# Optimization experiments

Measured on AMD Instinct MI355X. Metric: run time of the kernel, lower is better.

## Reference

```python
import jax, jax.numpy as jnp
import numpy as np

N_ATOMS = 51
VMIN = -10.0
VMAX = 10.0
GAMMA = 0.99
ACTION_DIM = 4
B = 524288

def setup_inputs() -> dict:
    key = jax.random.key(0)
    k1, k2, k3, k4, k5 = jax.random.split(key, 5)
    return {
        "next_logits": jax.random.normal(k1, (B, N_ATOMS), dtype=jnp.float32),
        "old_logits": jax.random.normal(k2, (B, ACTION_DIM, N_ATOMS), dtype=jnp.float32),
        "reward": jax.random.normal(k3, (B,), dtype=jnp.float32),
        "done": jax.random.uniform(k4, (B,), dtype=jnp.float32),
        "actions": jax.random.randint(k5, (B,), 0, ACTION_DIM, dtype=jnp.int32),
    }

def reference(next_logits, old_logits, reward, done, actions):
    b_sz, n_atoms = next_logits.shape
    delta_z = (VMAX - VMIN) / (n_atoms - 1)
    support = VMIN + delta_z * jnp.arange(n_atoms, dtype=next_logits.dtype)  # [A]
    # next-state distribution (Qnet softmax output), action-selected upstream
    next_p = jax.nn.softmax(next_logits, axis=-1)                            # [B, A]
    done_b = (done > 0.95).astype(next_logits.dtype)                         # binarize
    # Bellman-backed atoms, clamped to support range
    t_z = reward[:, None] + (1.0 - done_b)[:, None] * GAMMA * support        # [B, A]
    t_z = jnp.clip(t_z, VMIN, VMAX)
    b = (t_z - VMIN) / delta_z                                               # [B, A]
    l = jnp.floor(b).astype(jnp.int32)
    u = jnp.ceil(b).astype(jnp.int32)
    rows = jnp.arange(b_sz, dtype=jnp.int32)[:, None]                        # [B, 1]
    lf = l.astype(b.dtype)
    uf = u.astype(b.dtype)
    proj_dist = (jnp.zeros((b_sz, n_atoms), dtype=next_p.dtype)
                 .at[rows, l].add(next_p * (uf - b))
                 .at[rows, u].add(next_p * (b - lf)))                         # [B, A]
    proj_dist = jax.lax.stop_gradient(proj_dist)
    # cross-entropy loss against current net's action-conditioned distribution
    log_p_all = jax.nn.log_softmax(old_logits, axis=-1)                      # [B, act, A]
    log_p = jnp.take_along_axis(log_p_all, actions[:, None, None], axis=1)[:, 0, :]  # [B, A]
    loss = -jnp.mean(jnp.sum(proj_dist * log_p, axis=1))
    return loss, proj_dist
```

## Files before the change

### kernel.cpp

```cpp
#include <hip/hip_runtime.h>
#include <math.h>

#define N_ATOMS 51
#define VMIN_F  (-10.0f)
#define VMAX_F  (10.0f)
#define GAMMA_F (0.99f)
#define ACT     4
#define BLOCK   256
#define WPB     (BLOCK / 64)

__device__ __forceinline__ float wred_max(float v) {
#pragma unroll
    for (int off = 32; off; off >>= 1) v = fmaxf(v, __shfl_xor(v, off, 64));
    return v;
}
__device__ __forceinline__ float wred_sum(float v) {
#pragma unroll
    for (int off = 32; off; off >>= 1) v += __shfl_xor(v, off, 64);
    return v;
}

__global__ __launch_bounds__(BLOCK) void c51_kernel(
    const float* __restrict__ next_logits,
    const float* __restrict__ old_logits,
    const float* __restrict__ reward,
    const float* __restrict__ done,
    const int*   __restrict__ actions,
    float* __restrict__ out,
    int B)
{
    __shared__ float bins[WPB][64];
    __shared__ float wacc[WPB];

    const int lane  = threadIdx.x & 63;
    const int wid   = threadIdx.x >> 6;
    const int gwave = (blockIdx.x * blockDim.x + threadIdx.x) >> 6;
    const int nwav  = (gridDim.x * blockDim.x) >> 6;

    const float delta_z = 0.4f;
    const bool  active  = lane < N_ATOMS;
    const float zj = __fadd_rn(VMIN_F, __fmul_rn(delta_z, (float)lane));

    float acc = 0.0f;

    const int iters = (B + nwav - 1) / nwav;
    for (int it = 0; it < iters; ++it) {
        const int  r     = gwave + it * nwav;
        const bool valid = r < B;

        float x = (valid && active) ? next_logits[(size_t)r * N_ATOMS + lane]
                                    : -INFINITY;
        float m = wred_max(x);
        float e = (valid && active) ? expf(__fsub_rn(x, m)) : 0.0f;
        float s = wred_sum(e);
        float p = valid ? __fdiv_rn(e, s) : 0.0f;

        float wl = 0.0f, wu = 0.0f;
        int   li = 0,    ui = 0;
        if (valid) {
            float rw = reward[r];
            float db = (done[r] > 0.95f) ? 1.0f : 0.0f;
            float s1 = __fmul_rn(__fsub_rn(1.0f, db), GAMMA_F);
            float tz = __fadd_rn(rw, __fmul_rn(s1, zj));
            tz = fminf(fmaxf(tz, VMIN_F), VMAX_F);
            float b  = __fdiv_rn(__fsub_rn(tz, VMIN_F), delta_z);
            float lf = floorf(b);
            float uf = ceilf(b);
            li = (int)lf;
            ui = (int)uf;
            wl = __fmul_rn(p, __fsub_rn(uf, b));
            wu = __fmul_rn(p, __fsub_rn(b, lf));
        }

        bins[wid][lane] = 0.0f;
        __syncthreads();
        if (valid && active) {
            atomicAdd(&bins[wid][li], wl);
            atomicAdd(&bins[wid][ui], wu);
        }
        __syncthreads();
        float proj = (valid && active) ? bins[wid][lane] : 0.0f;

        float term = 0.0f;
        if (valid) {
            int a = actions[r];
            const float* op = old_logits + ((size_t)r * ACT + a) * N_ATOMS;
            float y  = active ? op[lane] : -INFINITY;
            float m2 = wred_max(y);
            float sh = __fsub_rn(y, m2);
            float e2 = active ? expf(sh) : 0.0f;
            float s2 = wred_sum(e2);
            float lp = __fsub_rn(sh, logf(s2));
            term = active ? __fmul_rn(proj, lp) : 0.0f;
        }
        acc += wred_sum(term);

        if (valid && active) out[1 + (size_t)r * N_ATOMS + lane] = proj;
    }

    if (lane == 0) wacc[wid] = acc;
    __syncthreads();
    if (threadIdx.x == 0) {
        float t = 0.0f;
#pragma unroll
        for (int i = 0; i < WPB; ++i) t += wacc[i];
        atomicAdd(out, -t / (float)B);
    }
}

extern "C" void kernel_launch(void* const* d_in, const int* in_sizes, int n_in,
                              void* d_out, int out_size, void* d_ws, size_t ws_size,
                              hipStream_t stream) {
    const float* next_logits = (const float*)d_in[0];
    const float* old_logits  = (const float*)d_in[1];
    const float* reward      = (const float*)d_in[2];
    const float* done        = (const float*)d_in[3];
    const int*   actions     = (const int*)d_in[4];
    float* out = (float*)d_out;
    const int B = in_sizes[2];

    hipMemsetAsync(d_out, 0, sizeof(float), stream);

    const int grid = 2048;
    c51_kernel<<<grid, BLOCK, 0, stream>>>(next_logits, old_logits, reward,
                                           done, actions, out, B);
}
```

Baseline: 986.1 us.

## Process two rows per wave with DPP reductions and wave-local LDS sync

Each wave now handles two rows per iteration and issues all global loads (logits, reward, done, actions, old logits) up front, so more memory requests are in flight at once. Shuffle-based reductions become DPP row operations plus a readlane. Block-wide __syncthreads around the per-wave histogram bins are replaced by lgkmcnt waits, since each wave owns its own bins. Fast __expf, __logf and rcp approximations replace the precise versions, and the loss is accumulated per lane with a single reduction at the end, at some cost in numerical accuracy.

Result: faster. 801.0 us (-18.8%).

```diff
diff --git a/kernel.cpp b/kernel.cpp
--- a/kernel.cpp
+++ b/kernel.cpp
@@ -8,16 +8,29 @@
 #define ACT     4
 #define BLOCK   256
 #define WPB     (BLOCK / 64)
+#define RPI     2
+#define GRID    2048
 
-__device__ __forceinline__ float wred_max(float v) {
-#pragma unroll
-    for (int off = 32; off; off >>= 1) v = fmaxf(v, __shfl_xor(v, off, 64));
-    return v;
+#define DPP_F(OLDF, SRCF, CTRL, RMASK) \
+  __int_as_float(__builtin_amdgcn_update_dpp(__float_as_int(OLDF), __float_as_int(SRCF), (CTRL), (RMASK), 0xF, false))
+
+__device__ __forceinline__ float wave_max_u(float v) {
+    v = fmaxf(v, DPP_F(-INFINITY, v, 0x111, 0xF));
+    v = fmaxf(v, DPP_F(-INFINITY, v, 0x112, 0xF));
+    v = fmaxf(v, DPP_F(-INFINITY, v, 0x114, 0xF));
+    v = fmaxf(v, DPP_F(-INFINITY, v, 0x118, 0xF));
+    v = fmaxf(v, DPP_F(-INFINITY, v, 0x142, 0xA));
+    v = fmaxf(v, DPP_F(-INFINITY, v, 0x143, 0xC));
+    return __int_as_float(__builtin_amdgcn_readlane(__float_as_int(v), 63));
 }
-__device__ __forceinline__ float wred_sum(float v) {
-#pragma unroll
-    for (int off = 32; off; off >>= 1) v += __shfl_xor(v, off, 64);
-    return v;
+__device__ __forceinline__ float wave_sum_u(float v) {
+    v = __fadd_rn(v, DPP_F(0.0f, v, 0x111, 0xF));
+    v = __fadd_rn(v, DPP_F(0.0f, v, 0x112, 0xF));
+    v = __fadd_rn(v, DPP_F(0.0f, v, 0x114, 0xF));
+    v = __fadd_rn(v, DPP_F(0.0f, v, 0x118, 0xF));
+    v = __fadd_rn(v, DPP_F(0.0f, v, 0x142, 0xA));
+    v = __fadd_rn(v, DPP_F(0.0f, v, 0x143, 0xC));
+    return __int_as_float(__builtin_amdgcn_readlane(__float_as_int(v), 63));
 }
 
 __global__ __launch_bounds__(BLOCK) void c51_kernel(
@@ -29,13 +42,13 @@
     float* __restrict__ out,
     int B)
 {
-    __shared__ float bins[WPB][64];
+    __shared__ float bins[WPB][RPI][64];
     __shared__ float wacc[WPB];
 
     const int lane  = threadIdx.x & 63;
     const int wid   = threadIdx.x >> 6;
-    const int gwave = (blockIdx.x * blockDim.x + threadIdx.x) >> 6;
-    const int nwav  = (gridDim.x * blockDim.x) >> 6;
+    const int gwave = blockIdx.x * WPB + wid;
+    const int nwav  = GRID * WPB;
 
     const float delta_z = 0.4f;
     const bool  active  = lane < N_ATOMS;
@@ -43,67 +56,87 @@
 
     float acc = 0.0f;
 
-    const int iters = (B + nwav - 1) / nwav;
+    const int stride = nwav * RPI;
+    const int iters  = (B + stride - 1) / stride;
+
     for (int it = 0; it < iters; ++it) {
-        const int  r     = gwave + it * nwav;
-        const bool valid = r < B;
+        const int  r0 = (gwave + it * nwav) * RPI;
+        const int  r1 = r0 + 1;
+        const bool vA = r0 < B, vB = r1 < B;
 
-        float x = (valid && active) ? next_logits[(size_t)r * N_ATOMS + lane]
-                                    : -INFINITY;
-        float m = wred_max(x);
-        float e = (valid && active) ? expf(__fsub_rn(x, m)) : 0.0f;
-        float s = wred_sum(e);
-        float p = valid ? __fdiv_rn(e, s) : 0.0f;
+        float xA = (vA && active) ? next_logits[(size_t)r0 * N_ATOMS + lane] : -INFINITY;
+        float xB = (vB && active) ? next_logits[(size_t)r1 * N_ATOMS + lane] : -INFINITY;
+        float rwA = vA ? reward[r0] : 0.0f;
+        float rwB = vB ? reward[r1] : 0.0f;
+        float dnA = vA ? done[r0] : 1.0f;
+        float dnB = vB ? done[r1] : 1.0f;
+        int   aA  = vA ? actions[r0] : 0;
+        int   aB  = vB ? actions[r1] : 0;
+        float yA = (vA && active) ? old_logits[((size_t)r0 * ACT + aA) * N_ATOMS + lane] : -INFINITY;
+        float yB = (vB && active) ? old_logits[((size_t)r1 * ACT + aB) * N_ATOMS + lane] : -INFINITY;
 
-        float wl = 0.0f, wu = 0.0f;
-        int   li = 0,    ui = 0;
-        if (valid) {
-            float rw = reward[r];
-            float db = (done[r] > 0.95f) ? 1.0f : 0.0f;
-            float s1 = __fmul_rn(__fsub_rn(1.0f, db), GAMMA_F);
-            float tz = __fadd_rn(rw, __fmul_rn(s1, zj));
-            tz = fminf(fmaxf(tz, VMIN_F), VMAX_F);
-            float b  = __fdiv_rn(__fsub_rn(tz, VMIN_F), delta_z);
-            float lf = floorf(b);
-            float uf = ceilf(b);
-            li = (int)lf;
-            ui = (int)uf;
-            wl = __fmul_rn(p, __fsub_rn(uf, b));
-            wu = __fmul_rn(p, __fsub_rn(b, lf));
+        float mA = wave_max_u(xA);
+        float mB = wave_max_u(xB);
+        float eA = (vA && active) ? __expf(__fsub_rn(xA, mA)) : 0.0f;
+        float eB = (vB && active) ? __expf(__fsub_rn(xB, mB)) : 0.0f;
+        float sA = wave_sum_u(eA);
+        float sB = wave_sum_u(eB);
+        float pA = __fmul_rn(eA, __builtin_amdgcn_rcpf(sA));
+        float pB = __fmul_rn(eB, __builtin_amdgcn_rcpf(sB));
+
+        float s1A = __fmul_rn(__fsub_rn(1.0f, (dnA > 0.95f) ? 1.0f : 0.0f), GAMMA_F);
+        float s1B = __fmul_rn(__fsub_rn(1.0f, (dnB > 0.95f) ? 1.0f : 0.0f), GAMMA_F);
+        float tzA = __fadd_rn(rwA, __fmul_rn(s1A, zj));
+        float tzB = __fadd_rn(rwB, __fmul_rn(s1B, zj));
+        tzA = fminf(fmaxf(tzA, VMIN_F), VMAX_F);
+        tzB = fminf(fmaxf(tzB, VMIN_F), VMAX_F);
+        float bA = __fdiv_rn(__fsub_rn(tzA, VMIN_F), delta_z);
+        float bB = __fdiv_rn(__fsub_rn(tzB, VMIN_F), delta_z);
+        float lfA = floorf(bA), ufA = ceilf(bA);
+        float lfB = floorf(bB), ufB = ceilf(bB);
+        int liA = (int)lfA, uiA = (int)ufA;
+        int liB = (int)lfB, uiB = (int)ufB;
+        float wlA = __fmul_rn(pA, __fsub_rn(ufA, bA));
+        float wuA = __fmul_rn(pA, __fsub_rn(bA, lfA));
+        float wlB = __fmul_rn(pB, __fsub_rn(ufB, bB));
+        float wuB = __fmul_rn(pB, __fsub_rn(bB, lfB));
+
+        bins[wid][0][lane] = 0.0f;
+        bins[wid][1][lane] = 0.0f;
+        asm volatile("s_waitcnt lgkmcnt(0)" ::: "memory");
+        if (active) {
+            if (vA) { atomicAdd(&bins[wid][0][liA], wlA); atomicAdd(&bins[wid][0][uiA], wuA); }
+            if (vB) { atomicAdd(&bins[wid][1][liB], wlB); atomicAdd(&bins[wid][1][uiB], wuB); }
         }
+        asm volatile("s_waitcnt lgkmcnt(0)" ::: "memory");
+        float prA = bins[wid][0][lane];
+        float prB = bins[wid][1][lane];
 
-        bins[wid][lane] = 0.0f;
-        __syncthreads();
-        if (valid && active) {
-            atomicAdd(&bins[wid][li], wl);
-            atomicAdd(&bins[wid][ui], wu);
-        }
-        __syncthreads();
-        float proj = (valid && active) ? bins[wid][lane] : 0.0f;
+        float m2A = wave_max_u(yA);
+        float m2B = wave_max_u(yB);
+        float shA = __fsub_rn(yA, m2A);
+        float shB = __fsub_rn(yB, m2B);
+        float e2A = (vA && active) ? __expf(shA) : 0.0f;
+        float e2B = (vB && active) ? __expf(shB) : 0.0f;
+        float s2A = wave_sum_u(e2A);
+        float s2B = wave_sum_u(e2B);
+        float lpA = __fsub_rn(shA, __logf(s2A));
+        float lpB = __fsub_rn(shB, __logf(s2B));
 
-        float term = 0.0f;
-        if (valid) {
-            int a = actions[r];
-            const float* op = old_logits + ((size_t)r * ACT + a) * N_ATOMS;
-            float y  = active ? op[lane] : -INFINITY;
-            float m2 = wred_max(y);
-            float sh = __fsub_rn(y, m2);
-            float e2 = active ? expf(sh) : 0.0f;
-            float s2 = wred_sum(e2);
-            float lp = __fsub_rn(sh, logf(s2));
-            term = active ? __fmul_rn(proj, lp) : 0.0f;
-        }
-        acc += wred_sum(term);
+        if (vA && active) acc = __fadd_rn(acc, __fmul_rn(prA, lpA));
+        if (vB && active) acc = __fadd_rn(acc, __fmul_rn(prB, lpB));
 
-        if (valid && active) out[1 + (size_t)r * N_ATOMS + lane] = proj;
+        if (vA && active) out[1 + (size_t)r0 * N_ATOMS + lane] = prA;
+        if (vB && active) out[1 + (size_t)r1 * N_ATOMS + lane] = prB;
     }
 
-    if (lane == 0) wacc[wid] = acc;
+    float tot = wave_sum_u(acc);
+    if (lane == 0) wacc[wid] = tot;
     __syncthreads();
     if (threadIdx.x == 0) {
         float t = 0.0f;
 #pragma unroll
-        for (int i = 0; i < WPB; ++i) t += wacc[i];
+        for (int i = 0; i < WPB; ++i) t = __fadd_rn(t, wacc[i]);
         atomicAdd(out, -t / (float)B);
     }
 }
@@ -121,7 +154,6 @@
 
     hipMemsetAsync(d_out, 0, sizeof(float), stream);
 
-    const int grid = 2048;
-    c51_kernel<<<grid, BLOCK, 0, stream>>>(next_logits, old_logits, reward,
+    c51_kernel<<<GRID, BLOCK, 0, stream>>>(next_logits, old_logits, reward,
                                            done, actions, out, B);
 }
```
